# Optimization experiments

Measured on AMD Instinct MI355X. Metric: run time of the kernel, lower is better.

The kernel has to match this reference:

```python
import jax, jax.numpy as jnp
import numpy as np

N_NODES = 50000
N_EDGES = 800000
D = 128
HEADS = 1
N_LAYERS = 3
NEG_SLOPE = 0.2


def setup_inputs() -> dict:
    key = jax.random.key(0)
    ks = jax.random.split(key, 8)
    x = jax.random.normal(ks[0], (N_NODES, D), dtype=jnp.float32)
    edge_index = jax.random.randint(ks[1], (2, N_EDGES), 0, N_NODES, dtype=jnp.int64)
    # Per-layer GATConv params (heads=1): lin [D, H*D], att_src/att_dst [H, D], bias [H*D]
    s = 1.0 / np.sqrt(D)
    W = jax.random.normal(ks[2], (N_LAYERS, D, HEADS * D), dtype=jnp.float32) * s
    att_src = jax.random.normal(ks[3], (N_LAYERS, HEADS, D), dtype=jnp.float32) * s
    att_dst = jax.random.normal(ks[4], (N_LAYERS, HEADS, D), dtype=jnp.float32) * s
    bias = jnp.zeros((N_LAYERS, HEADS * D), dtype=jnp.float32)
    return {"x": x, "edge_index": edge_index, "W": W, "att_src": att_src,
            "att_dst": att_dst, "bias": bias}


def _gat_conv(x, src, dst, W, a_src, a_dst, b):
    # x: [N, D] -> xp: [N, H, C]
    N = x.shape[0]
    xp = (x @ W).reshape(N, HEADS, D)
    alpha_s = jnp.sum(xp * a_src, axis=-1)  # [N, H]
    alpha_d = jnp.sum(xp * a_dst, axis=-1)  # [N, H]
    # per-edge attention logits (message j=src -> i=dst)
    e = alpha_s[src] + alpha_d[dst]                       # [E, H]
    e = jnp.where(e > 0, e, NEG_SLOPE * e)                # leaky_relu(0.2)
    # segment softmax over destination node
    m = jax.ops.segment_max(e, dst, num_segments=N)       # [N, H]
    ex = jnp.exp(e - m[dst])
    denom = jax.ops.segment_sum(ex, dst, num_segments=N)  # [N, H]
    coef = ex / (denom[dst] + 1e-16)                      # [E, H]
    # scatter-aggregate messages
    out = jax.ops.segment_sum(xp[src] * coef[:, :, None], dst, num_segments=N)  # [N, H, C]
    return out.reshape(N, HEADS * D) + b


def reference(x, edge_index, W, att_src, att_dst, bias):
    N = x.shape[0]
    # GATConv default add_self_loops=True: append (i, i) for every node
    loops = jnp.arange(N, dtype=edge_index.dtype)
    src = jnp.concatenate([edge_index[0], loops])
    dst = jnp.concatenate([edge_index[1], loops])
    h = x
    for l in range(N_LAYERS):
        # dropout omitted for deterministic reference (eval-mode semantics)
        h = _gat_conv(h, src, dst, W[l], att_src[l], att_dst[l], bias[l])
        if l < N_LAYERS - 1:
            h = jax.nn.gelu(h)
    return h
```

## Files before the change

### kernel.cpp

```cpp
#include <hip/hip_runtime.h>
#include <hip/hip_bf16.h>
#include <hip/hip_fp16.h>

#define NN    50000
#define NE    800000
#define ETOT  (NE + NN)
#define D     128
#define NB    ((NN + 255) / 256)
#define EB    ((ETOT + 255) / 256)
#define XB    ((NN * 64) / 256)

typedef _Float16 f16x8 __attribute__((ext_vector_type(8)));
typedef float    f32x4 __attribute__((ext_vector_type(4)));

__device__ __forceinline__ float gelu_fast(float x) {
    float x2 = x * x;
    float z2 = x * fmaf(x2, 0.07135483f, 1.5957691f);
    float e  = __expf(z2);
    return x - __fdividef(x, e + 1.0f);
}


__global__ __launch_bounds__(256) void prep_k(
        const int* __restrict__ dst_arr, int* __restrict__ counts, int* __restrict__ rank,
        const float* __restrict__ x, __half* __restrict__ xh,
        const float* __restrict__ W, __half* __restrict__ WT,
        const float* __restrict__ asrc, const float* __restrict__ adst,
        float* __restrict__ wasd) {
    int b = blockIdx.x, t = threadIdx.x;
    if (b < EB) {
        int e = b * 256 + t;
        if (e < ETOT) {
            int d = (e < NE) ? dst_arr[e] : (e - NE);
            rank[e] = atomicAdd(&counts[d], 1);
        }
    } else if (b < EB + XB) {
        int i = (b - EB) * 256 + t;
        float2 v = ((const float2*)x)[i];
        ((__half2*)xh)[i] = __floats2half2_rn(v.x, v.y);
    } else if (b < EB + XB + 192) {
        int i = (b - EB - XB) * 256 + t;
        int l = i >> 14, r = i & 16383;
        int k = r >> 7, c = r & 127;
        WT[(size_t)l * 16384 + (size_t)c * 128 + k] =
            __float2half_rn(W[(size_t)l * 16384 + (size_t)k * 128 + c]);
    } else {
        int l = b - EB - XB - 192;
        int k = t & 127, which = t >> 7;
        const float* wr = W + (size_t)l * 16384 + (size_t)k * 128;
        const float* av = (which ? adst : asrc) + (size_t)l * 128;
        float s = 0.f;
        #pragma unroll 4
        for (int c = 0; c < 128; ++c) s += wr[c] * av[c];
        wasd[l * 256 + which * 128 + k] = s;
    }
}


__global__ void scan1_k(const int* __restrict__ counts, int* __restrict__ blk_sums) {
    __shared__ int sm[4];
    int i = blockIdx.x * 256 + threadIdx.x;
    int v = (i < NN) ? counts[i] : 0;
    #pragma unroll
    for (int o = 32; o; o >>= 1) v += __shfl_xor(v, o);
    if ((threadIdx.x & 63) == 0) sm[threadIdx.x >> 6] = v;
    __syncthreads();
    if (threadIdx.x == 0) blk_sums[blockIdx.x] = sm[0] + sm[1] + sm[2] + sm[3];
}

__global__ void scan23_k(const int* __restrict__ counts, const int* __restrict__ blk_sums,
                         int* __restrict__ row_ptr) {
    __shared__ int s[256];
    __shared__ int boff_sh;
    int t = threadIdx.x, bid = blockIdx.x;
    if (t < 64) {
        int acc = 0;
        for (int i = t; i < bid; i += 64) acc += blk_sums[i];
        #pragma unroll
        for (int o = 32; o; o >>= 1) acc += __shfl_xor(acc, o);
        if (t == 0) boff_sh = acc;
    }
    __syncthreads();
    int boff = boff_sh;
    int i = bid * 256 + t;
    int v = (i < NN) ? counts[i] : 0;
    s[t] = v;
    __syncthreads();
    for (int off = 1; off < 256; off <<= 1) {
        int x = (t >= off) ? s[t - off] : 0;
        __syncthreads();
        s[t] += x;
        __syncthreads();
    }
    int excl = s[t] - v + boff;
    if (i < NN) row_ptr[i] = excl;
    if (bid == NB - 1 && t == 255) row_ptr[NN] = s[255] + boff;
}

__global__ void scatter2_k(const int* __restrict__ srcarr, const int* __restrict__ dstarr,
                           const int* __restrict__ rank, const int* __restrict__ row_ptr,
                           int* __restrict__ srcs) {
    int e = blockIdx.x * blockDim.x + threadIdx.x;
    if (e >= ETOT) return;
    int d, s;
    if (e < NE) { d = dstarr[e]; s = srcarr[e]; }
    else        { d = e - NE;    s = e - NE; }
    srcs[row_ptr[d] + rank[e]] = s;
}


__global__ __launch_bounds__(256) void gemm_mfma_k(
        const __half* __restrict__ TH, const __half* __restrict__ WT,
        const float* __restrict__ wasd,
        __half* __restrict__ XP, float* __restrict__ alpha_s, float* __restrict__ alpha_d) {
    __shared__ __half Bs[D * D];
    int t = threadIdx.x;
    #pragma unroll
    for (int it = 0; it < 8; ++it) {
        int b = it * 4096 + t * 16;
        int c = b >> 8;
        int swz = b ^ ((c & 7) << 4);
        *(uint4*)((char*)Bs + swz) = *(const uint4*)((const char*)WT + b);
    }
    __syncthreads();

    int w = t >> 6, lane = t & 63;
    int r0 = (blockIdx.x >> 1) * 256 + w * 64;
    int c0 = (blockIdx.x & 1) * 64;
    int lr = lane & 15, lg = lane >> 4;
    bool doalpha = (blockIdx.x & 1) == 0;

    f32x4 acc[4][4];
    #pragma unroll
    for (int i = 0; i < 4; ++i)
        #pragma unroll
        for (int j = 0; j < 4; ++j)
            acc[i][j] = (f32x4){0.f, 0.f, 0.f, 0.f};

    float ps[4] = {0, 0, 0, 0}, pd[4] = {0, 0, 0, 0};

    const char* abase = (const char*)TH;
    #pragma unroll
    for (int ks = 0; ks < 4; ++ks) {
        f16x8 bf[4];
        #pragma unroll
        for (int ct = 0; ct < 4; ++ct) {
            int c  = c0 + ct * 16 + lr;
            int kb = ks * 64 + lg * 16;
            int addr = c * 256 + (kb ^ ((c & 7) << 4));
            bf[ct] = *(const f16x8*)((const char*)Bs + addr);
        }
        float4 s0, s1, d0, d1;
        if (doalpha) {
            const float* wsp = wasd + ks * 32 + lg * 8;
            s0 = *(const float4*)(wsp);       s1 = *(const float4*)(wsp + 4);
            d0 = *(const float4*)(wsp + 128); d1 = *(const float4*)(wsp + 132);
        }
        #pragma unroll
        for (int rt = 0; rt < 4; ++rt) {
            int row = r0 + rt * 16 + lr;
            int rc  = row < NN ? row : NN - 1;
            f16x8 af = *(const f16x8*)(abase + (size_t)rc * 256 + ks * 64 + lg * 16);
            if (doalpha) {
                float a0 = (float)af[0], a1 = (float)af[1], a2 = (float)af[2], a3 = (float)af[3];
                float a4 = (float)af[4], a5 = (float)af[5], a6 = (float)af[6], a7 = (float)af[7];
                ps[rt] += a0*s0.x + a1*s0.y + a2*s0.z + a3*s0.w
                        + a4*s1.x + a5*s1.y + a6*s1.z + a7*s1.w;
                pd[rt] += a0*d0.x + a1*d0.y + a2*d0.z + a3*d0.w
                        + a4*d1.x + a5*d1.y + a6*d1.z + a7*d1.w;
            }
            #pragma unroll
            for (int ct = 0; ct < 4; ++ct)
                acc[rt][ct] = __builtin_amdgcn_mfma_f32_16x16x32_f16(
                                  af, bf[ct], acc[rt][ct], 0, 0, 0);
        }
    }

    #pragma unroll
    for (int rt = 0; rt < 4; ++rt) {
        #pragma unroll
        for (int q = 0; q < 4; ++q) {
            int row = r0 + rt * 16 + lg * 4 + q;
            if (row < NN) {
                #pragma unroll
                for (int ct = 0; ct < 4; ++ct) {
                    int col = c0 + ct * 16 + lr;
                    XP[(size_t)row * D + col] = __float2half_rn(acc[rt][ct][q]);
                }
            }
        }
    }

    if (doalpha) {
        #pragma unroll
        for (int rt = 0; rt < 4; ++rt) {
            float p = ps[rt], dq = pd[rt];
            p  += __shfl_xor(p, 16);  p  += __shfl_xor(p, 32);
            dq += __shfl_xor(dq, 16); dq += __shfl_xor(dq, 32);
            int row = r0 + rt * 16 + lr;
            if (lane < 16 && row < NN) { alpha_s[row] = p; alpha_d[row] = dq; }
        }
    }
}


template <int OUT32, int GELU>
__global__ __launch_bounds__(256) void agg_u_k(
        const int* __restrict__ row_ptr, const int* __restrict__ srcs,
        const float* __restrict__ alpha_s, const float* __restrict__ alpha_d,
        const __half* __restrict__ XPH, const float* __restrict__ bias,
        void* __restrict__ outp) {
    __shared__ float xch[4][128];
    int wv = threadIdx.x >> 6;
    int n = (blockIdx.x * blockDim.x + threadIdx.x) >> 6;
    int lane = threadIdx.x & 63;
    int beg = row_ptr[n], end = row_ptr[n + 1], deg = end - beg;
    float ad = alpha_d[n];
    int qw = lane >> 4, q = lane & 15;

    float2 fin;

    if (deg <= 64) {
        int sreg = 0;
        float e = -3.4e38f;
        if (lane < deg) {
            sreg = srcs[beg + lane];
            float v = alpha_s[sreg] + ad;
            e = v > 0.f ? v : 0.2f * v;
        }
        float m = e;
        #pragma unroll
        for (int o = 32; o; o >>= 1) m = fmaxf(m, __shfl_xor(m, o));
        float w = (lane < deg) ? __expf(e - m) : 0.f;
        float denom = w;
        #pragma unroll
        for (int o = 32; o; o >>= 1) denom += __shfl_xor(denom, o);

        float acc[8] = {0,0,0,0,0,0,0,0};
        int dgr = (deg + 3) & ~3;
        const char* xb = (const char*)XPH;
        int qb = q << 4;
        int j = 0;
        #define PROC(UU, WW)                                                     \
            {                                                                    \
                union { uint4 u; __half2 h[4]; } U; U.u = (UU);                  \
                float2 f0 = __half22float2(U.h[0]);                              \
                float2 f1 = __half22float2(U.h[1]);                              \
                float2 f2 = __half22float2(U.h[2]);                              \
                float2 f3 = __half22float2(U.h[3]);                              \
                acc[0] += (WW)*f0.x; acc[1] += (WW)*f0.y;                        \
                acc[2] += (WW)*f1.x; acc[3] += (WW)*f1.y;                        \
                acc[4] += (WW)*f2.x; acc[5] += (WW)*f2.y;                        \
                acc[6] += (WW)*f3.x; acc[7] += (WW)*f3.y;                        \
            }
        for (; j + 16 <= dgr; j += 16) {
            int   s0 = __shfl(sreg, j + qw);       float w0 = __shfl(w, j + qw);
            int   s1 = __shfl(sreg, j + 4 + qw);   float w1 = __shfl(w, j + 4 + qw);
            int   s2 = __shfl(sreg, j + 8 + qw);   float w2 = __shfl(w, j + 8 + qw);
            int   s3 = __shfl(sreg, j + 12 + qw);  float w3 = __shfl(w, j + 12 + qw);
            uint4 u0 = *(const uint4*)(xb + ((s0 << 8) + qb));
            uint4 u1 = *(const uint4*)(xb + ((s1 << 8) + qb));
            uint4 u2 = *(const uint4*)(xb + ((s2 << 8) + qb));
            uint4 u3 = *(const uint4*)(xb + ((s3 << 8) + qb));
            PROC(u0, w0) PROC(u1, w1) PROC(u2, w2) PROC(u3, w3)
        }
        for (; j < dgr; j += 4) {
            int   s0 = __shfl(sreg, j + qw);
            float w0 = __shfl(w, j + qw);
            uint4 u0 = *(const uint4*)(xb + ((s0 << 8) + qb));
            PROC(u0, w0)
        }
        #undef PROC
        #pragma unroll
        for (int f = 0; f < 8; ++f) {
            acc[f] += __shfl_xor(acc[f], 16);
            acc[f] += __shfl_xor(acc[f], 32);
        }
        if (lane < 16) {
            float4* p = (float4*)&xch[wv][q * 8];
            p[0] = make_float4(acc[0], acc[1], acc[2], acc[3]);
            p[1] = make_float4(acc[4], acc[5], acc[6], acc[7]);
        }
        __asm__ volatile("s_waitcnt lgkmcnt(0)" ::: "memory");
        __builtin_amdgcn_sched_barrier(0);
        float2 a2 = *(const float2*)&xch[wv][2 * lane];
        float inv = 1.f / (denom + 1e-16f);
        fin.x = a2.x * inv;
        fin.y = a2.y * inv;
    } else {
        float m = -3.4e38f;
        for (int i = beg + lane; i < end; i += 64) {
            int s = srcs[i];
            float v = alpha_s[s] + ad; v = v > 0.f ? v : 0.2f * v;
            m = fmaxf(m, v);
        }
        #pragma unroll
        for (int o = 32; o; o >>= 1) m = fmaxf(m, __shfl_xor(m, o));
        float denom = 0.f;
        for (int i = beg + lane; i < end; i += 64) {
            int s = srcs[i];
            float v = alpha_s[s] + ad; v = v > 0.f ? v : 0.2f * v;
            denom += __expf(v - m);
        }
        #pragma unroll
        for (int o = 32; o; o >>= 1) denom += __shfl_xor(denom, o);
        float2 acc = {0.f, 0.f};
        for (int i = beg; i < end; ++i) {
            int s = srcs[i];
            float v = alpha_s[s] + ad; v = v > 0.f ? v : 0.2f * v;
            float wgt = __expf(v - m);
            union { unsigned int x; __half2 h; } U;
            U.x = ((const unsigned int*)(XPH + (size_t)s * D))[lane];
            float2 f = __half22float2(U.h);
            acc.x += wgt * f.x; acc.y += wgt * f.y;
        }
        float inv = 1.f / (denom + 1e-16f);
        fin.x = acc.x * inv;
        fin.y = acc.y * inv;
    }

    float2 b2 = ((const float2*)bias)[lane];
    fin.x += b2.x;
    fin.y += b2.y;
    if (GELU) { fin.x = gelu_fast(fin.x); fin.y = gelu_fast(fin.y); }

    if (OUT32) {
        ((float2*)((float*)outp + (size_t)n * D))[lane] = fin;
    } else {
        ((__half2*)((__half*)outp + (size_t)n * D))[lane] = __floats2half2_rn(fin.x, fin.y);
    }
}


extern "C" void kernel_launch(void* const* d_in, const int* in_sizes, int n_in,
                              void* d_out, int out_size, void* d_ws, size_t ws_size,
                              hipStream_t stream) {
    const float* x    = (const float*)d_in[0];
    const int*   ei   = (const int*)d_in[1];
    const float* W    = (const float*)d_in[2];
    const float* asrc = (const float*)d_in[3];
    const float* adst = (const float*)d_in[4];
    const float* bias = (const float*)d_in[5];
    float* out = (float*)d_out;

    const int* src_arr = ei;
    const int* dst_arr = ei + NE;

    char* ws = (char*)d_ws;
    size_t off = 0;
    auto alloc = [&](size_t bytes) { char* p = ws + off; off += (bytes + 255) & ~(size_t)255; return p; };
    __half* th_a    = (__half*)alloc((size_t)NN * D * sizeof(__half));
    __half* th_b    = (__half*)alloc((size_t)NN * D * sizeof(__half));
    __half* xph     = (__half*)alloc((size_t)NN * D * sizeof(__half));
    __half* wt      = (__half*)alloc((size_t)3 * D * D * sizeof(__half));
    float*  as_a    = (float*)alloc(NN * sizeof(float));
    float*  ad_a    = (float*)alloc(NN * sizeof(float));
    float*  wasd    = (float*)alloc(3 * 256 * sizeof(float));
    int* counts    = (int*)alloc(NN * sizeof(int));
    int* row_ptr   = (int*)alloc((NN + 1) * sizeof(int));
    int* rank      = (int*)alloc((size_t)ETOT * sizeof(int));
    int* blk_sums  = (int*)alloc(NB * sizeof(int));
    int* srcs      = (int*)alloc((size_t)ETOT * sizeof(int));
    (void)ws_size; (void)in_sizes; (void)n_in; (void)out_size;

    hipMemsetAsync(counts, 0, NN * sizeof(int), stream);
    prep_k<<<EB + XB + 192 + 3, 256, 0, stream>>>(dst_arr, counts, rank,
                                                  x, th_a, W, wt, asrc, adst, wasd);
    scan1_k<<<NB, 256, 0, stream>>>(counts, blk_sums);
    scan23_k<<<NB, 256, 0, stream>>>(counts, blk_sums, row_ptr);
    scatter2_k<<<EB, 256, 0, stream>>>(src_arr, dst_arr, rank, row_ptr, srcs);

    int gb = 2 * ((NN + 255) / 256);
    int ab = NN / 4;

    gemm_mfma_k<<<gb, 256, 0, stream>>>(th_a, wt, wasd, xph, as_a, ad_a);
    agg_u_k<0, 1><<<ab, 256, 0, stream>>>(row_ptr, srcs, as_a, ad_a, xph, bias, th_b);
    gemm_mfma_k<<<gb, 256, 0, stream>>>(th_b, wt + 16384, wasd + 256, xph, as_a, ad_a);
    agg_u_k<0, 1><<<ab, 256, 0, stream>>>(row_ptr, srcs, as_a, ad_a, xph, bias + D, th_a);
    gemm_mfma_k<<<gb, 256, 0, stream>>>(th_a, wt + 32768, wasd + 512, xph, as_a, ad_a);
    agg_u_k<1, 0><<<ab, 256, 0, stream>>>(row_ptr, srcs, as_a, ad_a, xph, bias + 2 * D, out);
}
```

Baseline: 212.7 us.

## Split GAT layers into weight, column-half gather, and fused GEMM-plus-weight kernels

Restructures the pipeline. Attention weights are precomputed into a per-edge table. Aggregation is split into two 64-column halves, with XP stored half-major and blocks mapped so each half stays on a group of XCDs. The next layer's alpha dot products are computed inside the gather from the activated output using W·a, so they are no longer computed in the GEMM. That GEMM is then run in the same launch as the weight-table computation, and the first GEMM reads fp32 x directly and runs alongside the counting pass. The aim is fewer launches, better L2 locality for the gather, and removing the softmax from the gather's critical loop. In exchange, a per-edge weight array must be written and read back, and the gather now runs twice as many blocks.

Measured after the change: 304.6 us. 1.43x slower.

```diff
diff --git a/kernel.cpp b/kernel.cpp
--- a/kernel.cpp
+++ b/kernel.cpp
@@ -8,7 +8,6 @@
 #define D     128
 #define NB    ((NN + 255) / 256)
 #define EB    ((ETOT + 255) / 256)
-#define XB    ((NN * 64) / 256)
 
 typedef _Float16 f16x8 __attribute__((ext_vector_type(8)));
 typedef float    f32x4 __attribute__((ext_vector_type(4)));
@@ -21,31 +20,17 @@
 }
 
 
-__global__ __launch_bounds__(256) void prep_k(
-        const int* __restrict__ dst_arr, int* __restrict__ counts, int* __restrict__ rank,
-        const float* __restrict__ x, __half* __restrict__ xh,
-        const float* __restrict__ W, __half* __restrict__ WT,
+__global__ __launch_bounds__(256) void init_k(
+        int* __restrict__ counts, const float* __restrict__ W,
         const float* __restrict__ asrc, const float* __restrict__ adst,
-        float* __restrict__ wasd) {
+        float* __restrict__ wasd, __half* __restrict__ WT,
+        float* __restrict__ asp1, float* __restrict__ adp1) {
     int b = blockIdx.x, t = threadIdx.x;
-    if (b < EB) {
-        int e = b * 256 + t;
-        if (e < ETOT) {
-            int d = (e < NE) ? dst_arr[e] : (e - NE);
-            rank[e] = atomicAdd(&counts[d], 1);
-        }
-    } else if (b < EB + XB) {
-        int i = (b - EB) * 256 + t;
-        float2 v = ((const float2*)x)[i];
-        ((__half2*)xh)[i] = __floats2half2_rn(v.x, v.y);
-    } else if (b < EB + XB + 192) {
-        int i = (b - EB - XB) * 256 + t;
-        int l = i >> 14, r = i & 16383;
-        int k = r >> 7, c = r & 127;
-        WT[(size_t)l * 16384 + (size_t)c * 128 + k] =
-            __float2half_rn(W[(size_t)l * 16384 + (size_t)k * 128 + c]);
-    } else {
-        int l = b - EB - XB - 192;
+    if (b < NB) {
+        int i = b * 256 + t;
+        if (i < NN) counts[i] = 0;
+    } else if (b < NB + 3) {
+        int l = b - NB;
         int k = t & 127, which = t >> 7;
         const float* wr = W + (size_t)l * 16384 + (size_t)k * 128;
         const float* av = (which ? adst : asrc) + (size_t)l * 128;
@@ -53,7 +38,222 @@
         #pragma unroll 4
         for (int c = 0; c < 128; ++c) s += wr[c] * av[c];
         wasd[l * 256 + which * 128 + k] = s;
-    }
+    } else if (b < NB + 3 + 192) {
+        int i = (b - NB - 3) * 256 + t;
+        int l = i >> 14, r = i & 16383;
+        int k = r >> 7, c = r & 127;
+        WT[(size_t)l * 16384 + (size_t)c * 128 + k] =
+            __float2half_rn(W[(size_t)l * 16384 + (size_t)k * 128 + c]);
+    } else {
+        int i = (b - NB - 3 - 192) * 256 + t;
+        if (i < NN) { asp1[i] = 0.f; adp1[i] = 0.f; }
+    }
+}
+
+
+template <int AIN32, int DOALPHA>
+__device__ __forceinline__ void gemm_body(
+        int b2, int t, const void* __restrict__ A, const __half* __restrict__ WT,
+        const float* __restrict__ wasd, __half* __restrict__ XPH,
+        float* __restrict__ asp, float* __restrict__ adp, __half* Bs) {
+    #pragma unroll
+    for (int it = 0; it < 8; ++it) {
+        int bb = it * 4096 + t * 16;
+        int c = bb >> 8;
+        int swz = bb ^ ((c & 7) << 4);
+        *(uint4*)((char*)Bs + swz) = *(const uint4*)((const char*)WT + bb);
+    }
+    __syncthreads();
+
+    int w = t >> 6, lane = t & 63;
+    int r0 = (b2 >> 1) * 256 + w * 64;
+    int c0 = (b2 & 1) * 64;
+    int lr = lane & 15, lg = lane >> 4;
+    bool doalpha = DOALPHA && (b2 & 1) == 0;
+
+    f32x4 acc[4][4];
+    #pragma unroll
+    for (int i = 0; i < 4; ++i)
+        #pragma unroll
+        for (int j = 0; j < 4; ++j)
+            acc[i][j] = (f32x4){0.f, 0.f, 0.f, 0.f};
+
+    float ps[4] = {0, 0, 0, 0}, pd[4] = {0, 0, 0, 0};
+
+    #pragma unroll
+    for (int ks = 0; ks < 4; ++ks) {
+        f16x8 bf[4];
+        #pragma unroll
+        for (int ct = 0; ct < 4; ++ct) {
+            int c  = c0 + ct * 16 + lr;
+            int kb = ks * 64 + lg * 16;
+            int addr = c * 256 + (kb ^ ((c & 7) << 4));
+            bf[ct] = *(const f16x8*)((const char*)Bs + addr);
+        }
+        float4 s0, s1, d0, d1;
+        if (doalpha) {
+            const float* wsp = wasd + ks * 32 + lg * 8;
+            s0 = *(const float4*)(wsp);       s1 = *(const float4*)(wsp + 4);
+            d0 = *(const float4*)(wsp + 128); d1 = *(const float4*)(wsp + 132);
+        }
+        #pragma unroll
+        for (int rt = 0; rt < 4; ++rt) {
+            int row = r0 + rt * 16 + lr;
+            int rc  = row < NN ? row : NN - 1;
+            f16x8 af;
+            float4 f0, f1;
+            if (AIN32) {
+                const float* ap = (const float*)A + (size_t)rc * D + ks * 32 + lg * 8;
+                f0 = *(const float4*)ap;
+                f1 = *(const float4*)(ap + 4);
+                af[0] = (_Float16)f0.x; af[1] = (_Float16)f0.y;
+                af[2] = (_Float16)f0.z; af[3] = (_Float16)f0.w;
+                af[4] = (_Float16)f1.x; af[5] = (_Float16)f1.y;
+                af[6] = (_Float16)f1.z; af[7] = (_Float16)f1.w;
+            } else {
+                af = *(const f16x8*)((const char*)A + (size_t)rc * 256 + ks * 64 + lg * 16);
+                if (doalpha) {
+                    f0 = make_float4((float)af[0], (float)af[1], (float)af[2], (float)af[3]);
+                    f1 = make_float4((float)af[4], (float)af[5], (float)af[6], (float)af[7]);
+                }
+            }
+            if (doalpha) {
+                ps[rt] += f0.x*s0.x + f0.y*s0.y + f0.z*s0.z + f0.w*s0.w
+                        + f1.x*s1.x + f1.y*s1.y + f1.z*s1.z + f1.w*s1.w;
+                pd[rt] += f0.x*d0.x + f0.y*d0.y + f0.z*d0.z + f0.w*d0.w
+                        + f1.x*d1.x + f1.y*d1.y + f1.z*d1.z + f1.w*d1.w;
+            }
+            #pragma unroll
+            for (int ct = 0; ct < 4; ++ct)
+                acc[rt][ct] = __builtin_amdgcn_mfma_f32_16x16x32_f16(
+                                  af, bf[ct], acc[rt][ct], 0, 0, 0);
+        }
+    }
+
+    __half* xpt = XPH + (size_t)(c0 >> 6) * NN * 64;
+    #pragma unroll
+    for (int rt = 0; rt < 4; ++rt) {
+        #pragma unroll
+        for (int q = 0; q < 4; ++q) {
+            int row = r0 + rt * 16 + lg * 4 + q;
+            if (row < NN) {
+                #pragma unroll
+                for (int ct = 0; ct < 4; ++ct)
+                    xpt[(size_t)row * 64 + ct * 16 + lr] = __float2half_rn(acc[rt][ct][q]);
+            }
+        }
+    }
+
+    if (doalpha) {
+        #pragma unroll
+        for (int rt = 0; rt < 4; ++rt) {
+            float p = ps[rt], dq = pd[rt];
+            p  += __shfl_xor(p, 16);  p  += __shfl_xor(p, 32);
+            dq += __shfl_xor(dq, 16); dq += __shfl_xor(dq, 32);
+            int row = r0 + rt * 16 + lr;
+            if (lane < 16 && row < NN) { asp[row] = p; adp[row] = dq; }
+        }
+    }
+}
+
+
+__device__ __forceinline__ void wgt_body(
+        int n, int lane, const int* __restrict__ row_ptr, const int* __restrict__ srcs,
+        const float* __restrict__ asp0, const float* __restrict__ asp1,
+        const float* __restrict__ adp0, const float* __restrict__ adp1,
+        float* __restrict__ w_tab) {
+    int beg = row_ptr[n], end = row_ptr[n + 1], deg = end - beg;
+    float ad = adp0[n] + adp1[n];
+    if (deg <= 64) {
+        float e = -3.4e38f;
+        if (lane < deg) {
+            int s = srcs[beg + lane];
+            float v = asp0[s] + asp1[s] + ad;
+            e = v > 0.f ? v : 0.2f * v;
+        }
+        float m = e;
+        #pragma unroll
+        for (int o = 32; o; o >>= 1) m = fmaxf(m, __shfl_xor(m, o));
+        float w = (lane < deg) ? __expf(e - m) : 0.f;
+        float denom = w;
+        #pragma unroll
+        for (int o = 32; o; o >>= 1) denom += __shfl_xor(denom, o);
+        float inv = 1.f / (denom + 1e-16f);
+        if (lane < deg) w_tab[beg + lane] = w * inv;
+    } else {
+        float m = -3.4e38f;
+        for (int i = beg + lane; i < end; i += 64) {
+            int s = srcs[i];
+            float v = asp0[s] + asp1[s] + ad;
+            v = v > 0.f ? v : 0.2f * v;
+            m = fmaxf(m, v);
+        }
+        #pragma unroll
+        for (int o = 32; o; o >>= 1) m = fmaxf(m, __shfl_xor(m, o));
+        float denom = 0.f;
+        for (int i = beg + lane; i < end; i += 64) {
+            int s = srcs[i];
+            float v = asp0[s] + asp1[s] + ad;
+            v = v > 0.f ? v : 0.2f * v;
+            denom += __expf(v - m);
+        }
+        #pragma unroll
+        for (int o = 32; o; o >>= 1) denom += __shfl_xor(denom, o);
+        float inv = 1.f / (denom + 1e-16f);
+        for (int i = beg + lane; i < end; i += 64) {
+            int s = srcs[i];
+            float v = asp0[s] + asp1[s] + ad;
+            v = v > 0.f ? v : 0.2f * v;
+            w_tab[i] = __expf(v - m) * inv;
+        }
+    }
+}
+
+
+__global__ __launch_bounds__(256) void prep2_k(
+        const int* __restrict__ dst_arr, int* __restrict__ counts, int* __restrict__ rank,
+        const float* __restrict__ x, const __half* __restrict__ WT,
+        const float* __restrict__ wasd, __half* __restrict__ XPH,
+        float* __restrict__ asp0, float* __restrict__ adp0) {
+    __shared__ __half Bs[D * D];
+    int b = blockIdx.x, t = threadIdx.x;
+    if (b < EB) {
+        int e = b * 256 + t;
+        if (e < ETOT) {
+            int d = (e < NE) ? dst_arr[e] : (e - NE);
+            rank[e] = atomicAdd(&counts[d], 1);
+        }
+    } else {
+        gemm_body<1, 1>(b - EB, t, x, WT, wasd, XPH, asp0, adp0, Bs);
+    }
+}
+
+
+__global__ __launch_bounds__(256) void gw_k(
+        const __half* __restrict__ TH, const __half* __restrict__ WT,
+        __half* __restrict__ XPH,
+        const int* __restrict__ row_ptr, const int* __restrict__ srcs,
+        const float* __restrict__ asp0, const float* __restrict__ asp1,
+        const float* __restrict__ adp0, const float* __restrict__ adp1,
+        float* __restrict__ w_tab) {
+    __shared__ __half Bs[D * D];
+    int b = blockIdx.x, t = threadIdx.x;
+    if (b < 392) {
+        gemm_body<0, 0>(b, t, TH, WT, nullptr, XPH, nullptr, nullptr, Bs);
+    } else {
+        int n = (b - 392) * 4 + (t >> 6);
+        wgt_body(n, t & 63, row_ptr, srcs, asp0, asp1, adp0, adp1, w_tab);
+    }
+}
+
+
+__global__ __launch_bounds__(256) void wgt_k(
+        const int* __restrict__ row_ptr, const int* __restrict__ srcs,
+        const float* __restrict__ asp0, const float* __restrict__ asp1,
+        const float* __restrict__ adp0, const float* __restrict__ adp1,
+        float* __restrict__ w_tab) {
+    int n = blockIdx.x * 4 + (threadIdx.x >> 6);
+    wgt_body(n, threadIdx.x & 63, row_ptr, srcs, asp0, asp1, adp0, adp1, w_tab);
 }
 
 
@@ -109,225 +309,69 @@
 }
 
 
-__global__ __launch_bounds__(256) void gemm_mfma_k(
-        const __half* __restrict__ TH, const __half* __restrict__ WT,
-        const float* __restrict__ wasd,
-        __half* __restrict__ XP, float* __restrict__ alpha_s, float* __restrict__ alpha_d) {
-    __shared__ __half Bs[D * D];
-    int t = threadIdx.x;
-    #pragma unroll
-    for (int it = 0; it < 8; ++it) {
-        int b = it * 4096 + t * 16;
-        int c = b >> 8;
-        int swz = b ^ ((c & 7) << 4);
-        *(uint4*)((char*)Bs + swz) = *(const uint4*)((const char*)WT + b);
-    }
-    __syncthreads();
-
-    int w = t >> 6, lane = t & 63;
-    int r0 = (blockIdx.x >> 1) * 256 + w * 64;
-    int c0 = (blockIdx.x & 1) * 64;
-    int lr = lane & 15, lg = lane >> 4;
-    bool doalpha = (blockIdx.x & 1) == 0;
-
-    f32x4 acc[4][4];
-    #pragma unroll
-    for (int i = 0; i < 4; ++i)
-        #pragma unroll
-        for (int j = 0; j < 4; ++j)
-            acc[i][j] = (f32x4){0.f, 0.f, 0.f, 0.f};
-
-    float ps[4] = {0, 0, 0, 0}, pd[4] = {0, 0, 0, 0};
-
-    const char* abase = (const char*)TH;
-    #pragma unroll
-    for (int ks = 0; ks < 4; ++ks) {
-        f16x8 bf[4];
-        #pragma unroll
-        for (int ct = 0; ct < 4; ++ct) {
-            int c  = c0 + ct * 16 + lr;
-            int kb = ks * 64 + lg * 16;
-            int addr = c * 256 + (kb ^ ((c & 7) << 4));
-            bf[ct] = *(const f16x8*)((const char*)Bs + addr);
-        }
-        float4 s0, s1, d0, d1;
-        if (doalpha) {
-            const float* wsp = wasd + ks * 32 + lg * 8;
-            s0 = *(const float4*)(wsp);       s1 = *(const float4*)(wsp + 4);
-            d0 = *(const float4*)(wsp + 128); d1 = *(const float4*)(wsp + 132);
-        }
-        #pragma unroll
-        for (int rt = 0; rt < 4; ++rt) {
-            int row = r0 + rt * 16 + lr;
-            int rc  = row < NN ? row : NN - 1;
-            f16x8 af = *(const f16x8*)(abase + (size_t)rc * 256 + ks * 64 + lg * 16);
-            if (doalpha) {
-                float a0 = (float)af[0], a1 = (float)af[1], a2 = (float)af[2], a3 = (float)af[3];
-                float a4 = (float)af[4], a5 = (float)af[5], a6 = (float)af[6], a7 = (float)af[7];
-                ps[rt] += a0*s0.x + a1*s0.y + a2*s0.z + a3*s0.w
-                        + a4*s1.x + a5*s1.y + a6*s1.z + a7*s1.w;
-                pd[rt] += a0*d0.x + a1*d0.y + a2*d0.z + a3*d0.w
-                        + a4*d1.x + a5*d1.y + a6*d1.z + a7*d1.w;
-            }
-            #pragma unroll
-            for (int ct = 0; ct < 4; ++ct)
-                acc[rt][ct] = __builtin_amdgcn_mfma_f32_16x16x32_f16(
-                                  af, bf[ct], acc[rt][ct], 0, 0, 0);
-        }
-    }
-
-    #pragma unroll
-    for (int rt = 0; rt < 4; ++rt) {
-        #pragma unroll
-        for (int q = 0; q < 4; ++q) {
-            int row = r0 + rt * 16 + lg * 4 + q;
-            if (row < NN) {
-                #pragma unroll
-                for (int ct = 0; ct < 4; ++ct) {
-                    int col = c0 + ct * 16 + lr;
-                    XP[(size_t)row * D + col] = __float2half_rn(acc[rt][ct][q]);
-                }
-            }
-        }
-    }
-
-    if (doalpha) {
-        #pragma unroll
-        for (int rt = 0; rt < 4; ++rt) {
-            float p = ps[rt], dq = pd[rt];
-            p  += __shfl_xor(p, 16);  p  += __shfl_xor(p, 32);
-            dq += __shfl_xor(dq, 16); dq += __shfl_xor(dq, 32);
-            int row = r0 + rt * 16 + lr;
-            if (lane < 16 && row < NN) { alpha_s[row] = p; alpha_d[row] = dq; }
-        }
-    }
-}
-
-
-template <int OUT32, int GELU>
-__global__ __launch_bounds__(256) void agg_u_k(
+template <int OUT32, int GELU, int HAS_NEXT>
+__global__ __launch_bounds__(256) void gath_k(
         const int* __restrict__ row_ptr, const int* __restrict__ srcs,
-        const float* __restrict__ alpha_s, const float* __restrict__ alpha_d,
-        const __half* __restrict__ XPH, const float* __restrict__ bias,
-        void* __restrict__ outp) {
-    __shared__ float xch[4][128];
-    int wv = threadIdx.x >> 6;
-    int n = (blockIdx.x * blockDim.x + threadIdx.x) >> 6;
-    int lane = threadIdx.x & 63;
+        const float* __restrict__ w_tab, const __half* __restrict__ XPH,
+        const float* __restrict__ bias, const float* __restrict__ wn,
+        void* __restrict__ outp, float* __restrict__ asp, float* __restrict__ adp) {
+    __shared__ float xch[4][64];
+    int b = blockIdx.x;
+    int xcd  = b & 7;
+    int half = xcd >> 2;
+    int lblk = (b >> 3) * 4 + (xcd & 3);
+    int wv = threadIdx.x >> 6, lane = threadIdx.x & 63;
+    int n = lblk * 4 + wv;
     int beg = row_ptr[n], end = row_ptr[n + 1], deg = end - beg;
-    float ad = alpha_d[n];
-    int qw = lane >> 4, q = lane & 15;
-
-    float2 fin;
-
-    if (deg <= 64) {
-        int sreg = 0;
-        float e = -3.4e38f;
-        if (lane < deg) {
-            sreg = srcs[beg + lane];
-            float v = alpha_s[sreg] + ad;
-            e = v > 0.f ? v : 0.2f * v;
-        }
-        float m = e;
-        #pragma unroll
-        for (int o = 32; o; o >>= 1) m = fmaxf(m, __shfl_xor(m, o));
-        float w = (lane < deg) ? __expf(e - m) : 0.f;
-        float denom = w;
-        #pragma unroll
-        for (int o = 32; o; o >>= 1) denom += __shfl_xor(denom, o);
-
-        float acc[8] = {0,0,0,0,0,0,0,0};
-        int dgr = (deg + 3) & ~3;
-        const char* xb = (const char*)XPH;
-        int qb = q << 4;
-        int j = 0;
-        #define PROC(UU, WW)                                                     \
-            {                                                                    \
-                union { uint4 u; __half2 h[4]; } U; U.u = (UU);                  \
-                float2 f0 = __half22float2(U.h[0]);                              \
-                float2 f1 = __half22float2(U.h[1]);                              \
-                float2 f2 = __half22float2(U.h[2]);                              \
-                float2 f3 = __half22float2(U.h[3]);                              \
-                acc[0] += (WW)*f0.x; acc[1] += (WW)*f0.y;                        \
-                acc[2] += (WW)*f1.x; acc[3] += (WW)*f1.y;                        \
-                acc[4] += (WW)*f2.x; acc[5] += (WW)*f2.y;                        \
-                acc[6] += (WW)*f3.x; acc[7] += (WW)*f3.y;                        \
-            }
-        for (; j + 16 <= dgr; j += 16) {
-            int   s0 = __shfl(sreg, j + qw);       float w0 = __shfl(w, j + qw);
-            int   s1 = __shfl(sreg, j + 4 + qw);   float w1 = __shfl(w, j + 4 + qw);
-            int   s2 = __shfl(sreg, j + 8 + qw);   float w2 = __shfl(w, j + 8 + qw);
-            int   s3 = __shfl(sreg, j + 12 + qw);  float w3 = __shfl(w, j + 12 + qw);
-            uint4 u0 = *(const uint4*)(xb + ((s0 << 8) + qb));
-            uint4 u1 = *(const uint4*)(xb + ((s1 << 8) + qb));
-            uint4 u2 = *(const uint4*)(xb + ((s2 << 8) + qb));
-            uint4 u3 = *(const uint4*)(xb + ((s3 << 8) + qb));
-            PROC(u0, w0) PROC(u1, w1) PROC(u2, w2) PROC(u3, w3)
-        }
-        for (; j < dgr; j += 4) {
-            int   s0 = __shfl(sreg, j + qw);
-            float w0 = __shfl(w, j + qw);
-            uint4 u0 = *(const uint4*)(xb + ((s0 << 8) + qb));
-            PROC(u0, w0)
-        }
-        #undef PROC
-        #pragma unroll
-        for (int f = 0; f < 8; ++f) {
-            acc[f] += __shfl_xor(acc[f], 16);
-            acc[f] += __shfl_xor(acc[f], 32);
-        }
-        if (lane < 16) {
-            float4* p = (float4*)&xch[wv][q * 8];
-            p[0] = make_float4(acc[0], acc[1], acc[2], acc[3]);
-            p[1] = make_float4(acc[4], acc[5], acc[6], acc[7]);
-        }
-        __asm__ volatile("s_waitcnt lgkmcnt(0)" ::: "memory");
-        __builtin_amdgcn_sched_barrier(0);
-        float2 a2 = *(const float2*)&xch[wv][2 * lane];
-        float inv = 1.f / (denom + 1e-16f);
-        fin.x = a2.x * inv;
-        fin.y = a2.y * inv;
-    } else {
-        float m = -3.4e38f;
-        for (int i = beg + lane; i < end; i += 64) {
-            int s = srcs[i];
-            float v = alpha_s[s] + ad; v = v > 0.f ? v : 0.2f * v;
-            m = fmaxf(m, v);
-        }
-        #pragma unroll
-        for (int o = 32; o; o >>= 1) m = fmaxf(m, __shfl_xor(m, o));
-        float denom = 0.f;
-        for (int i = beg + lane; i < end; i += 64) {
-            int s = srcs[i];
-            float v = alpha_s[s] + ad; v = v > 0.f ? v : 0.2f * v;
-            denom += __expf(v - m);
-        }
-        #pragma unroll
-        for (int o = 32; o; o >>= 1) denom += __shfl_xor(denom, o);
-        float2 acc = {0.f, 0.f};
-        for (int i = beg; i < end; ++i) {
-            int s = srcs[i];
-            float v = alpha_s[s] + ad; v = v > 0.f ? v : 0.2f * v;
-            float wgt = __expf(v - m);
-            union { unsigned int x; __half2 h; } U;
-            U.x = ((const unsigned int*)(XPH + (size_t)s * D))[lane];
-            float2 f = __half22float2(U.h);
-            acc.x += wgt * f.x; acc.y += wgt * f.y;
-        }
-        float inv = 1.f / (denom + 1e-16f);
-        fin.x = acc.x * inv;
-        fin.y = acc.y * inv;
-    }
-
-    float2 b2 = ((const float2*)bias)[lane];
-    fin.x += b2.x;
-    fin.y += b2.y;
-    if (GELU) { fin.x = gelu_fast(fin.x); fin.y = gelu_fast(fin.y); }
-
-    if (OUT32) {
-        ((float2*)((float*)outp + (size_t)n * D))[lane] = fin;
-    } else {
-        ((__half2*)((__half*)outp + (size_t)n * D))[lane] = __floats2half2_rn(fin.x, fin.y);
+    const char* tb = (const char*)(XPH + (size_t)half * NN * 64);
+    int og = lane >> 3, qb = (lane & 7) << 4;
+
+    float acc[8] = {0, 0, 0, 0, 0, 0, 0, 0};
+    for (int j = 0; j < deg; j += 8) {
+        int idx = beg + j + og;
+        int cidx = idx < end - 1 ? idx : end - 1;
+        int   s = srcs[cidx];
+        float w = (j + og < deg) ? w_tab[cidx] : 0.f;
+        uint4 u = *(const uint4*)(tb + ((s << 7) + qb));
+        union { uint4 uu; __half2 h[4]; } U; U.uu = u;
+        float2 f0 = __half22float2(U.h[0]);
+        float2 f1 = __half22float2(U.h[1]);
+        float2 f2 = __half22float2(U.h[2]);
+        float2 f3 = __half22float2(U.h[3]);
+        acc[0] += w * f0.x; acc[1] += w * f0.y;
+        acc[2] += w * f1.x; acc[3] += w * f1.y;
+        acc[4] += w * f2.x; acc[5] += w * f2.y;
+        acc[6] += w * f3.x; acc[7] += w * f3.y;
+    }
+    #pragma unroll
+    for (int f = 0; f < 8; ++f) {
+        acc[f] += __shfl_xor(acc[f], 8);
+        acc[f] += __shfl_xor(acc[f], 16);
+        acc[f] += __shfl_xor(acc[f], 32);
+    }
+    if (lane < 8) {
+        float4* p = (float4*)&xch[wv][lane * 8];
+        p[0] = make_float4(acc[0], acc[1], acc[2], acc[3]);
+        p[1] = make_float4(acc[4], acc[5], acc[6], acc[7]);
+    }
+    __asm__ volatile("s_waitcnt lgkmcnt(0)" ::: "memory");
+    __builtin_amdgcn_sched_barrier(0);
+    float fin = xch[wv][lane];
+
+    fin += bias[half * 64 + lane];
+    if (GELU) fin = gelu_fast(fin);
+    if (OUT32) ((float*)outp)[(size_t)n * D + half * 64 + lane] = fin;
+    else       ((__half*)outp)[(size_t)n * D + half * 64 + lane] = __float2half_rn(fin);
+
+    if (HAS_NEXT) {
+        float ps = fin * wn[half * 64 + lane];
+        float pd = fin * wn[128 + half * 64 + lane];
+        #pragma unroll
+        for (int o = 32; o; o >>= 1) {
+            ps += __shfl_xor(ps, o);
+            pd += __shfl_xor(pd, o);
+        }
+        if (lane == 0) { asp[(size_t)half * NN + n] = ps; adp[(size_t)half * NN + n] = pd; }
     }
 }
 
@@ -351,10 +395,11 @@
     auto alloc = [&](size_t bytes) { char* p = ws + off; off += (bytes + 255) & ~(size_t)255; return p; };
     __half* th_a    = (__half*)alloc((size_t)NN * D * sizeof(__half));
     __half* th_b    = (__half*)alloc((size_t)NN * D * sizeof(__half));
-    __half* xph     = (__half*)alloc((size_t)NN * D * sizeof(__half));
+    __half* xph     = (__half*)alloc((size_t)2 * NN * 64 * sizeof(__half));
     __half* wt      = (__half*)alloc((size_t)3 * D * D * sizeof(__half));
-    float*  as_a    = (float*)alloc(NN * sizeof(float));
-    float*  ad_a    = (float*)alloc(NN * sizeof(float));
+    float*  w_tab   = (float*)alloc((size_t)ETOT * sizeof(float));
+    float*  asp     = (float*)alloc((size_t)2 * NN * sizeof(float));
+    float*  adp     = (float*)alloc((size_t)2 * NN * sizeof(float));
     float*  wasd    = (float*)alloc(3 * 256 * sizeof(float));
     int* counts    = (int*)alloc(NN * sizeof(int));
     int* row_ptr   = (int*)alloc((NN + 1) * sizeof(int));
@@ -363,20 +408,24 @@
     int* srcs      = (int*)alloc((size_t)ETOT * sizeof(int));
     (void)ws_size; (void)in_sizes; (void)n_in; (void)out_size;
 
-    hipMemsetAsync(counts, 0, NN * sizeof(int), stream);
-    prep_k<<<EB + XB + 192 + 3, 256, 0, stream>>>(dst_arr, counts, rank,
-                                                  x, th_a, W, wt, asrc, adst, wasd);
+    init_k<<<NB + 3 + 192 + NB, 256, 0, stream>>>(counts, W, asrc, adst, wasd, wt,
+                                                  asp + NN, adp + NN);
+    prep2_k<<<EB + 392, 256, 0, stream>>>(dst_arr, counts, rank, x, wt, wasd,
+                                          xph, asp, adp);
     scan1_k<<<NB, 256, 0, stream>>>(counts, blk_sums);
     scan23_k<<<NB, 256, 0, stream>>>(counts, blk_sums, row_ptr);
     scatter2_k<<<EB, 256, 0, stream>>>(src_arr, dst_arr, rank, row_ptr, srcs);
 
-    int gb = 2 * ((NN + 255) / 256);
-    int ab = NN / 4;
-
-    gemm_mfma_k<<<gb, 256, 0, stream>>>(th_a, wt, wasd, xph, as_a, ad_a);
-    agg_u_k<0, 1><<<ab, 256, 0, stream>>>(row_ptr, srcs, as_a, ad_a, xph, bias, th_b);
-    gemm_mfma_k<<<gb, 256, 0, stream>>>(th_b, wt + 16384, wasd + 256, xph, as_a, ad_a);
-    agg_u_k<0, 1><<<ab, 256, 0, stream>>>(row_ptr, srcs, as_a, ad_a, xph, bias + D, th_a);
-    gemm_mfma_k<<<gb, 256, 0, stream>>>(th_a, wt + 32768, wasd + 512, xph, as_a, ad_a);
-    agg_u_k<1, 0><<<ab, 256, 0, stream>>>(row_ptr, srcs, as_a, ad_a, xph, bias + 2 * D, out);
-}
+    wgt_k<<<NN / 4, 256, 0, stream>>>(row_ptr, srcs, asp, asp + NN, adp, adp + NN, w_tab);
+    gath_k<0, 1, 1><<<2 * NN / 4, 256, 0, stream>>>(row_ptr, srcs, w_tab, xph,
+                                                    bias, wasd + 256, th_b, asp, adp);
+    gw_k<<<392 + NN / 4, 256, 0, stream>>>(th_b, wt + 16384, xph, row_ptr, srcs,
+                                           asp, asp + NN, adp, adp + NN, w_tab);
+    gath_k<0, 1, 1><<<2 * NN / 4, 256, 0, stream>>>(row_ptr, srcs, w_tab, xph,
+                                                    bias + D, wasd + 512, th_a, asp, adp);
+    gw_k<<<392 + NN / 4, 256, 0, stream>>>(th_a, wt + 32768, xph, row_ptr, srcs,
+                                           asp, asp + NN, adp, adp + NN, w_tab);
+    gath_k<1, 0, 0><<<2 * NN / 4, 256, 0, stream>>>(row_ptr, srcs, w_tab, xph,
+                                                    bias + 2 * D, nullptr, out,
+                                                    nullptr, nullptr);
+}
```

## Fuse first-layer GEMM with edge counting and read fp32 input directly

Applied to the files above, without the earlier changes.

Removes the separate fp32-to-fp16 conversion of x and the standalone first-layer GEMM launch. The first GEMM now reads x in fp32 and converts it in registers, and runs in the same launch as the edge-count atomics. The memset is replaced by a zeroing section in a new init kernel that also builds WT and wasd. This saves one full pass over x and one launch. The cost is a heavier mixed kernel with 32 KB of LDS per block even for the atomic-counting blocks, which can lower their occupancy.

New measurement: 205.2 us. 1.04x faster.

```diff
diff --git a/kernel.cpp b/kernel.cpp
--- a/kernel.cpp
+++ b/kernel.cpp
@@ -8,7 +8,6 @@
 #define D     128
 #define NB    ((NN + 255) / 256)
 #define EB    ((ETOT + 255) / 256)
-#define XB    ((NN * 64) / 256)
 
 typedef _Float16 f16x8 __attribute__((ext_vector_type(8)));
 typedef float    f32x4 __attribute__((ext_vector_type(4)));
@@ -21,31 +20,16 @@
 }
 
 
-__global__ __launch_bounds__(256) void prep_k(
-        const int* __restrict__ dst_arr, int* __restrict__ counts, int* __restrict__ rank,
-        const float* __restrict__ x, __half* __restrict__ xh,
-        const float* __restrict__ W, __half* __restrict__ WT,
+__global__ __launch_bounds__(256) void init_k(
+        int* __restrict__ counts, const float* __restrict__ W,
         const float* __restrict__ asrc, const float* __restrict__ adst,
-        float* __restrict__ wasd) {
+        float* __restrict__ wasd, __half* __restrict__ WT) {
     int b = blockIdx.x, t = threadIdx.x;
-    if (b < EB) {
-        int e = b * 256 + t;
-        if (e < ETOT) {
-            int d = (e < NE) ? dst_arr[e] : (e - NE);
-            rank[e] = atomicAdd(&counts[d], 1);
-        }
-    } else if (b < EB + XB) {
-        int i = (b - EB) * 256 + t;
-        float2 v = ((const float2*)x)[i];
-        ((__half2*)xh)[i] = __floats2half2_rn(v.x, v.y);
-    } else if (b < EB + XB + 192) {
-        int i = (b - EB - XB) * 256 + t;
-        int l = i >> 14, r = i & 16383;
-        int k = r >> 7, c = r & 127;
-        WT[(size_t)l * 16384 + (size_t)c * 128 + k] =
-            __float2half_rn(W[(size_t)l * 16384 + (size_t)k * 128 + c]);
-    } else {
-        int l = b - EB - XB - 192;
+    if (b < NB) {
+        int i = b * 256 + t;
+        if (i < NN) counts[i] = 0;
+    } else if (b < NB + 3) {
+        int l = b - NB;
         int k = t & 127, which = t >> 7;
         const float* wr = W + (size_t)l * 16384 + (size_t)k * 128;
         const float* av = (which ? adst : asrc) + (size_t)l * 128;
@@ -53,7 +37,146 @@
         #pragma unroll 4
         for (int c = 0; c < 128; ++c) s += wr[c] * av[c];
         wasd[l * 256 + which * 128 + k] = s;
-    }
+    } else {
+        int i = (b - NB - 3) * 256 + t;
+        int l = i >> 14, r = i & 16383;
+        int k = r >> 7, c = r & 127;
+        WT[(size_t)l * 16384 + (size_t)c * 128 + k] =
+            __float2half_rn(W[(size_t)l * 16384 + (size_t)k * 128 + c]);
+    }
+}
+
+
+template <int AIN32>
+__device__ __forceinline__ void gemm_body(
+        int b2, int t, const void* __restrict__ A, const __half* __restrict__ WT,
+        const float* __restrict__ wasd, __half* __restrict__ XP,
+        float* __restrict__ alpha_s, float* __restrict__ alpha_d, __half* Bs) {
+    #pragma unroll
+    for (int it = 0; it < 8; ++it) {
+        int bb = it * 4096 + t * 16;
+        int c = bb >> 8;
+        int swz = bb ^ ((c & 7) << 4);
+        *(uint4*)((char*)Bs + swz) = *(const uint4*)((const char*)WT + bb);
+    }
+    __syncthreads();
+
+    int w = t >> 6, lane = t & 63;
+    int r0 = (b2 >> 1) * 256 + w * 64;
+    int c0 = (b2 & 1) * 64;
+    int lr = lane & 15, lg = lane >> 4;
+    bool doalpha = (b2 & 1) == 0;
+
+    f32x4 acc[4][4];
+    #pragma unroll
+    for (int i = 0; i < 4; ++i)
+        #pragma unroll
+        for (int j = 0; j < 4; ++j)
+            acc[i][j] = (f32x4){0.f, 0.f, 0.f, 0.f};
+
+    float ps[4] = {0, 0, 0, 0}, pd[4] = {0, 0, 0, 0};
+
+    #pragma unroll
+    for (int ks = 0; ks < 4; ++ks) {
+        f16x8 bf[4];
+        #pragma unroll
+        for (int ct = 0; ct < 4; ++ct) {
+            int c  = c0 + ct * 16 + lr;
+            int kb = ks * 64 + lg * 16;
+            int addr = c * 256 + (kb ^ ((c & 7) << 4));
+            bf[ct] = *(const f16x8*)((const char*)Bs + addr);
+        }
+        float4 s0, s1, d0, d1;
+        if (doalpha) {
+            const float* wsp = wasd + ks * 32 + lg * 8;
+            s0 = *(const float4*)(wsp);       s1 = *(const float4*)(wsp + 4);
+            d0 = *(const float4*)(wsp + 128); d1 = *(const float4*)(wsp + 132);
+        }
+        #pragma unroll
+        for (int rt = 0; rt < 4; ++rt) {
+            int row = r0 + rt * 16 + lr;
+            int rc  = row < NN ? row : NN - 1;
+            f16x8 af;
+            float4 f0, f1;
+            if (AIN32) {
+                const float* ap = (const float*)A + (size_t)rc * D + ks * 32 + lg * 8;
+                f0 = *(const float4*)ap;
+                f1 = *(const float4*)(ap + 4);
+                af[0] = (_Float16)f0.x; af[1] = (_Float16)f0.y;
+                af[2] = (_Float16)f0.z; af[3] = (_Float16)f0.w;
+                af[4] = (_Float16)f1.x; af[5] = (_Float16)f1.y;
+                af[6] = (_Float16)f1.z; af[7] = (_Float16)f1.w;
+            } else {
+                af = *(const f16x8*)((const char*)A + (size_t)rc * 256 + ks * 64 + lg * 16);
+                if (doalpha) {
+                    f0 = make_float4((float)af[0], (float)af[1], (float)af[2], (float)af[3]);
+                    f1 = make_float4((float)af[4], (float)af[5], (float)af[6], (float)af[7]);
+                }
+            }
+            if (doalpha) {
+                ps[rt] += f0.x*s0.x + f0.y*s0.y + f0.z*s0.z + f0.w*s0.w
+                        + f1.x*s1.x + f1.y*s1.y + f1.z*s1.z + f1.w*s1.w;
+                pd[rt] += f0.x*d0.x + f0.y*d0.y + f0.z*d0.z + f0.w*d0.w
+                        + f1.x*d1.x + f1.y*d1.y + f1.z*d1.z + f1.w*d1.w;
+            }
+            #pragma unroll
+            for (int ct = 0; ct < 4; ++ct)
+                acc[rt][ct] = __builtin_amdgcn_mfma_f32_16x16x32_f16(
+                                  af, bf[ct], acc[rt][ct], 0, 0, 0);
+        }
+    }
+
+    #pragma unroll
+    for (int rt = 0; rt < 4; ++rt) {
+        #pragma unroll
+        for (int q = 0; q < 4; ++q) {
+            int row = r0 + rt * 16 + lg * 4 + q;
+            if (row < NN) {
+                #pragma unroll
+                for (int ct = 0; ct < 4; ++ct)
+                    XP[(size_t)row * D + c0 + ct * 16 + lr] = __float2half_rn(acc[rt][ct][q]);
+            }
+        }
+    }
+
+    if (doalpha) {
+        #pragma unroll
+        for (int rt = 0; rt < 4; ++rt) {
+            float p = ps[rt], dq = pd[rt];
+            p  += __shfl_xor(p, 16);  p  += __shfl_xor(p, 32);
+            dq += __shfl_xor(dq, 16); dq += __shfl_xor(dq, 32);
+            int row = r0 + rt * 16 + lr;
+            if (lane < 16 && row < NN) { alpha_s[row] = p; alpha_d[row] = dq; }
+        }
+    }
+}
+
+
+__global__ __launch_bounds__(256) void prep2_k(
+        const int* __restrict__ dst_arr, int* __restrict__ counts, int* __restrict__ rank,
+        const float* __restrict__ x, const __half* __restrict__ WT,
+        const float* __restrict__ wasd, __half* __restrict__ XPH,
+        float* __restrict__ alpha_s, float* __restrict__ alpha_d) {
+    __shared__ __half Bs[D * D];
+    int b = blockIdx.x, t = threadIdx.x;
+    if (b < EB) {
+        int e = b * 256 + t;
+        if (e < ETOT) {
+            int d = (e < NE) ? dst_arr[e] : (e - NE);
+            rank[e] = atomicAdd(&counts[d], 1);
+        }
+    } else {
+        gemm_body<1>(b - EB, t, x, WT, wasd, XPH, alpha_s, alpha_d, Bs);
+    }
+}
+
+
+__global__ __launch_bounds__(256) void gemm_k(
+        const __half* __restrict__ TH, const __half* __restrict__ WT,
+        const float* __restrict__ wasd, __half* __restrict__ XPH,
+        float* __restrict__ alpha_s, float* __restrict__ alpha_d) {
+    __shared__ __half Bs[D * D];
+    gemm_body<0>(blockIdx.x, threadIdx.x, TH, WT, wasd, XPH, alpha_s, alpha_d, Bs);
 }
 
 
@@ -106,101 +229,6 @@
     if (e < NE) { d = dstarr[e]; s = srcarr[e]; }
     else        { d = e - NE;    s = e - NE; }
     srcs[row_ptr[d] + rank[e]] = s;
-}
-
-
-__global__ __launch_bounds__(256) void gemm_mfma_k(
-        const __half* __restrict__ TH, const __half* __restrict__ WT,
-        const float* __restrict__ wasd,
-        __half* __restrict__ XP, float* __restrict__ alpha_s, float* __restrict__ alpha_d) {
-    __shared__ __half Bs[D * D];
-    int t = threadIdx.x;
-    #pragma unroll
-    for (int it = 0; it < 8; ++it) {
-        int b = it * 4096 + t * 16;
-        int c = b >> 8;
-        int swz = b ^ ((c & 7) << 4);
-        *(uint4*)((char*)Bs + swz) = *(const uint4*)((const char*)WT + b);
-    }
-    __syncthreads();
-
-    int w = t >> 6, lane = t & 63;
-    int r0 = (blockIdx.x >> 1) * 256 + w * 64;
-    int c0 = (blockIdx.x & 1) * 64;
-    int lr = lane & 15, lg = lane >> 4;
-    bool doalpha = (blockIdx.x & 1) == 0;
-
-    f32x4 acc[4][4];
-    #pragma unroll
-    for (int i = 0; i < 4; ++i)
-        #pragma unroll
-        for (int j = 0; j < 4; ++j)
-            acc[i][j] = (f32x4){0.f, 0.f, 0.f, 0.f};
-
-    float ps[4] = {0, 0, 0, 0}, pd[4] = {0, 0, 0, 0};
-
-    const char* abase = (const char*)TH;
-    #pragma unroll
-    for (int ks = 0; ks < 4; ++ks) {
-        f16x8 bf[4];
-        #pragma unroll
-        for (int ct = 0; ct < 4; ++ct) {
-            int c  = c0 + ct * 16 + lr;
-            int kb = ks * 64 + lg * 16;
-            int addr = c * 256 + (kb ^ ((c & 7) << 4));
-            bf[ct] = *(const f16x8*)((const char*)Bs + addr);
-        }
-        float4 s0, s1, d0, d1;
-        if (doalpha) {
-            const float* wsp = wasd + ks * 32 + lg * 8;
-            s0 = *(const float4*)(wsp);       s1 = *(const float4*)(wsp + 4);
-            d0 = *(const float4*)(wsp + 128); d1 = *(const float4*)(wsp + 132);
-        }
-        #pragma unroll
-        for (int rt = 0; rt < 4; ++rt) {
-            int row = r0 + rt * 16 + lr;
-            int rc  = row < NN ? row : NN - 1;
-            f16x8 af = *(const f16x8*)(abase + (size_t)rc * 256 + ks * 64 + lg * 16);
-            if (doalpha) {
-                float a0 = (float)af[0], a1 = (float)af[1], a2 = (float)af[2], a3 = (float)af[3];
-                float a4 = (float)af[4], a5 = (float)af[5], a6 = (float)af[6], a7 = (float)af[7];
-                ps[rt] += a0*s0.x + a1*s0.y + a2*s0.z + a3*s0.w
-                        + a4*s1.x + a5*s1.y + a6*s1.z + a7*s1.w;
-                pd[rt] += a0*d0.x + a1*d0.y + a2*d0.z + a3*d0.w
-                        + a4*d1.x + a5*d1.y + a6*d1.z + a7*d1.w;
-            }
-            #pragma unroll
-            for (int ct = 0; ct < 4; ++ct)
-                acc[rt][ct] = __builtin_amdgcn_mfma_f32_16x16x32_f16(
-                                  af, bf[ct], acc[rt][ct], 0, 0, 0);
-        }
-    }
-
-    #pragma unroll
-    for (int rt = 0; rt < 4; ++rt) {
-        #pragma unroll
-        for (int q = 0; q < 4; ++q) {
-            int row = r0 + rt * 16 + lg * 4 + q;
-            if (row < NN) {
-                #pragma unroll
-                for (int ct = 0; ct < 4; ++ct) {
-                    int col = c0 + ct * 16 + lr;
-                    XP[(size_t)row * D + col] = __float2half_rn(acc[rt][ct][q]);
-                }
-            }
-        }
-    }
-
-    if (doalpha) {
-        #pragma unroll
-        for (int rt = 0; rt < 4; ++rt) {
-            float p = ps[rt], dq = pd[rt];
-            p  += __shfl_xor(p, 16);  p  += __shfl_xor(p, 32);
-            dq += __shfl_xor(dq, 16); dq += __shfl_xor(dq, 32);
-            int row = r0 + rt * 16 + lr;
-            if (lane < 16 && row < NN) { alpha_s[row] = p; alpha_d[row] = dq; }
-        }
-    }
 }
 
 
@@ -363,20 +391,18 @@
     int* srcs      = (int*)alloc((size_t)ETOT * sizeof(int));
     (void)ws_size; (void)in_sizes; (void)n_in; (void)out_size;
 
-    hipMemsetAsync(counts, 0, NN * sizeof(int), stream);
-    prep_k<<<EB + XB + 192 + 3, 256, 0, stream>>>(dst_arr, counts, rank,
-                                                  x, th_a, W, wt, asrc, adst, wasd);
+    init_k<<<NB + 3 + 192, 256, 0, stream>>>(counts, W, asrc, adst, wasd, wt);
+    prep2_k<<<EB + 392, 256, 0, stream>>>(dst_arr, counts, rank, x, wt, wasd,
+                                          xph, as_a, ad_a);
     scan1_k<<<NB, 256, 0, stream>>>(counts, blk_sums);
     scan23_k<<<NB, 256, 0, stream>>>(counts, blk_sums, row_ptr);
     scatter2_k<<<EB, 256, 0, stream>>>(src_arr, dst_arr, rank, row_ptr, srcs);
 
-    int gb = 2 * ((NN + 255) / 256);
     int ab = NN / 4;
 
-    gemm_mfma_k<<<gb, 256, 0, stream>>>(th_a, wt, wasd, xph, as_a, ad_a);
     agg_u_k<0, 1><<<ab, 256, 0, stream>>>(row_ptr, srcs, as_a, ad_a, xph, bias, th_b);
-    gemm_mfma_k<<<gb, 256, 0, stream>>>(th_b, wt + 16384, wasd + 256, xph, as_a, ad_a);
+    gemm_k<<<392, 256, 0, stream>>>(th_b, wt + 16384, wasd + 256, xph, as_a, ad_a);
     agg_u_k<0, 1><<<ab, 256, 0, stream>>>(row_ptr, srcs, as_a, ad_a, xph, bias + D, th_a);
-    gemm_mfma_k<<<gb, 256, 0, stream>>>(th_a, wt + 32768, wasd + 512, xph, as_a, ad_a);
+    gemm_k<<<392, 256, 0, stream>>>(th_a, wt + 32768, wasd + 512, xph, as_a, ad_a);
     agg_u_k<1, 0><<<ab, 256, 0, stream>>>(row_ptr, srcs, as_a, ad_a, xph, bias + 2 * D, out);
 }
```
